# Kernel tuning notes

Hardware: AMD Instinct MI355X
Metric: run time of the kernel (lower is better)

## Reference

```python
import jax, jax.numpy as jnp
import numpy as np

N_NODES = 200000
D_IN = 256
D_OUT = 256
B = 4096
K1 = 25   # layer-1 fanout
K2 = 10   # layer-2 fanout
M = B * (1 + K2)  # layer-1 node set size: batch centers + their sampled neighbors


def setup_inputs() -> dict:
    key = jax.random.key(0)
    k1, k2, k3, k4, k5, k6 = jax.random.split(key, 6)
    features = jax.random.normal(k1, (N_NODES, D_IN), dtype=jnp.float32)
    # SageLayer weights: [out, 2*in] (concat path, gcn=False); small kaiming-like scale
    W1 = jax.random.normal(k2, (D_OUT, 2 * D_IN), dtype=jnp.float32) * 0.05
    W2 = jax.random.normal(k3, (D_OUT, 2 * D_OUT), dtype=jnp.float32) * 0.05
    nodes_batch = jax.random.randint(k4, (B,), 0, N_NODES, dtype=jnp.int64)
    neigh2 = jax.random.randint(k5, (B, K2), 0, N_NODES, dtype=jnp.int64)
    neigh1 = jax.random.randint(k6, (M, K1), 0, N_NODES, dtype=jnp.int64)
    return {"features": features, "W1": W1, "W2": W2,
            "nodes_batch": nodes_batch, "neigh2": neigh2, "neigh1": neigh1}


def reference(features, W1, W2, nodes_batch, neigh2, neigh1):
    # Layer-1 node set: centers first, then their sampled layer-2 neighbors.
    l1_nodes = jnp.concatenate([nodes_batch, neigh2.reshape(-1)])  # [M]
    # ---- layer 1: MEAN aggregate over K1 sampled neighbors (gather + mean) ----
    agg1 = jnp.mean(features[neigh1], axis=1)          # [M, K1, D_IN] -> [M, D_IN]
    self1 = features[l1_nodes]                         # [M, D_IN]
    # SageLayer: relu(W.mm(cat(self, agg).T)).T == relu(cat @ W.T)
    h1 = jax.nn.relu(jnp.concatenate([self1, agg1], axis=1) @ W1.T)  # [M, D_OUT]
    # ---- layer 2: centers are h1[:B]; neighbor embeddings are h1[B:] in blocks of K2 ----
    nb = nodes_batch.shape[0]
    agg2 = jnp.mean(h1[nb:].reshape(nb, -1, h1.shape[1]), axis=1)    # [B, D_OUT]
    h2 = jax.nn.relu(jnp.concatenate([h1[:nb], agg2], axis=1) @ W2.T)  # [B, D_OUT]
    return h2
```

## Files before the change

### kernel.cpp

```cpp
#include <hip/hip_runtime.h>
#include <hip/hip_bf16.h>

typedef __attribute__((ext_vector_type(8))) short bf16x8;
typedef __attribute__((ext_vector_type(4))) float f32x4;
typedef __attribute__((ext_vector_type(2))) float f32x2;

#define B_SZ   4096
#define K1     25
#define K2     10
#define M_L1   45056
#define D      256
#define K_DIM  512
#define N_NODES 200000

#define AS1 __attribute__((address_space(1)))
#define AS3 __attribute__((address_space(3)))

static __device__ __forceinline__ unsigned short f2bf(float f) {
    union { float f; unsigned u; } v; v.f = f;
    return (unsigned short)((v.u + 0x7fffu + ((v.u >> 16) & 1u)) >> 16);
}
static __device__ __forceinline__ float bf2f(unsigned short h) {
    union { unsigned u; float f; } v; v.u = ((unsigned)h) << 16;
    return v.f;
}

__global__ __launch_bounds__(256)
void convert_all(const float* __restrict__ f, unsigned* __restrict__ f8,
                 const float* __restrict__ W1, const float* __restrict__ W2,
                 unsigned short* __restrict__ W1b, unsigned short* __restrict__ W2b) {
    const size_t i = ((size_t)blockIdx.x * 256 + threadIdx.x) * 8;
    const float4 a = *(const float4*)(f + i);
    const float4 b = *(const float4*)(f + i + 4);
    unsigned u0 = 0, u1 = 0;
    u0 = __builtin_amdgcn_cvt_pk_fp8_f32(a.x, a.y, u0, false);
    u0 = __builtin_amdgcn_cvt_pk_fp8_f32(a.z, a.w, u0, true);
    u1 = __builtin_amdgcn_cvt_pk_fp8_f32(b.x, b.y, u1, false);
    u1 = __builtin_amdgcn_cvt_pk_fp8_f32(b.z, b.w, u1, true);
    uint2 r; r.x = u0; r.y = u1;
    *(uint2*)(f8 + (i >> 2)) = r;
    const int j = blockIdx.x * 256 + threadIdx.x;
    if (j < D * K_DIM) {
        W1b[j] = f2bf(W1[j]);
        W2b[j] = f2bf(W2[j]);
    }
}

__global__ __launch_bounds__(512)
void fused_l1(const float* __restrict__ feat,
              const unsigned* __restrict__ f8,
              const int* __restrict__ nodes_batch,
              const int* __restrict__ neigh2,
              const int* __restrict__ neigh1,
              const unsigned short* __restrict__ W,
              unsigned short* __restrict__ h1) {
    __shared__ unsigned short As[64 * 512];
    __shared__ unsigned short Bs[2][256 * 64];
    const int tid  = threadIdx.x;
    const int w    = tid >> 6, lane = tid & 63;
    const int quad = lane >> 4, l16 = lane & 15;
    const size_t row0 = (size_t)blockIdx.x * 64;

    const int srow   = lane >> 3;
    const int schunk = ((lane & 7) ^ srow) << 3;
    const unsigned short* bG = W + (size_t)srow * K_DIM + schunk;

    #pragma unroll
    for (int c = w; c < 32; c += 8)
        __builtin_amdgcn_global_load_lds(
            (const AS1 void*)(bG + (size_t)(c * 8) * K_DIM),
            (AS3 void*)(&Bs[0][c * 512]), 16, 0, 0);

    #pragma unroll 2
    for (int rr = 0; rr < 8; ++rr) {
        const int r = (w << 3) + rr;
        const int m = (int)row0 + r;
        const int self_node = (m < B_SZ) ? nodes_batch[m] : neigh2[m - B_SZ];
        const int* nb = neigh1 + (size_t)m * K1;
        int idxv = (lane < K1) ? nb[lane] : 0;
        const float4 s = *(const float4*)(feat + (size_t)self_node * D + (lane << 2));
        unsigned q[K1];
        #pragma unroll
        for (int j = 0; j < K1; ++j) {
            const int node = __shfl(idxv, j);
            q[j] = f8[(size_t)node * (D / 4) + lane];
        }
        float a0 = 0.f, a1 = 0.f, a2 = 0.f, a3 = 0.f;
        #pragma unroll
        for (int j = 0; j < K1; ++j) {
            const f32x2 lo = __builtin_amdgcn_cvt_pk_f32_fp8(q[j], false);
            const f32x2 hi = __builtin_amdgcn_cvt_pk_f32_fp8(q[j], true);
            a0 += lo.x; a1 += lo.y; a2 += hi.x; a3 += hi.y;
        }
        const float inv = 1.0f / (float)K1;
        const int e0 = lane << 2;
        const int p0 = (e0 >> 3) ^ (r & 7);
        *(ushort4*)&As[r * 512 + (p0 << 3) + (e0 & 7)] =
            make_ushort4(f2bf(s.x), f2bf(s.y), f2bf(s.z), f2bf(s.w));
        const int e1 = D + (lane << 2);
        const int p1 = (e1 >> 3) ^ (r & 7);
        *(ushort4*)&As[r * 512 + (p1 << 3) + (e1 & 7)] =
            make_ushort4(f2bf(a0 * inv), f2bf(a1 * inv), f2bf(a2 * inv), f2bf(a3 * inv));
    }

    asm volatile("s_waitcnt vmcnt(0)" ::: "memory");
    __syncthreads();

    const int wm = (w >> 2) << 5;
    const int wn = (w & 3) << 6;
    f32x4 acc[2][4];
    #pragma unroll
    for (int i = 0; i < 2; ++i)
        #pragma unroll
        for (int j = 0; j < 4; ++j)
            acc[i][j] = (f32x4){0.f, 0.f, 0.f, 0.f};

    for (int t = 0; t < 8; ++t) {
        if (t < 7) {
            #pragma unroll
            for (int c = w; c < 32; c += 8)
                __builtin_amdgcn_global_load_lds(
                    (const AS1 void*)(bG + (size_t)(c * 8) * K_DIM + ((t + 1) << 6)),
                    (AS3 void*)(&Bs[(t + 1) & 1][c * 512]), 16, 0, 0);
        }
        #pragma unroll
        for (int ks = 0; ks < 2; ++ks) {
            bf16x8 af[2], bfr[4];
            #pragma unroll
            for (int i = 0; i < 2; ++i) {
                const int row = wm + i * 16 + l16;
                const int ch  = (t << 3) + (ks << 2) + quad;
                af[i] = *(const bf16x8*)&As[row * 512 + ((ch ^ (row & 7)) << 3)];
            }
            #pragma unroll
            for (int i = 0; i < 4; ++i) {
                const int row = wn + i * 16 + l16;
                bfr[i] = *(const bf16x8*)&Bs[t & 1][row * 64 + ((((ks << 2) + quad) ^ (l16 & 7)) << 3)];
            }
            #pragma unroll
            for (int mi = 0; mi < 2; ++mi)
                #pragma unroll
                for (int ni = 0; ni < 4; ++ni)
                    acc[mi][ni] = __builtin_amdgcn_mfma_f32_16x16x32_bf16(
                        af[mi], bfr[ni], acc[mi][ni], 0, 0, 0);
        }
        asm volatile("s_waitcnt vmcnt(0)" ::: "memory");
        __syncthreads();
    }

    #pragma unroll
    for (int mi = 0; mi < 2; ++mi)
        #pragma unroll
        for (int ni = 0; ni < 4; ++ni)
            #pragma unroll
            for (int rg = 0; rg < 4; ++rg) {
                const size_t gm = row0 + wm + mi * 16 + quad * 4 + rg;
                const size_t gn = (size_t)wn + ni * 16 + l16;
                float v = acc[mi][ni][rg];
                v = v > 0.f ? v : 0.f;
                h1[gm * D + gn] = f2bf(v);
            }
}

__global__ __launch_bounds__(256)
void fused_l2(const unsigned short* __restrict__ h1,
              const unsigned short* __restrict__ W,
              float* __restrict__ out) {
    __shared__ unsigned short As[16 * 512];
    __shared__ unsigned short Bs[2][256 * 64];
    const int tid  = threadIdx.x;
    const int w    = tid >> 6, lane = tid & 63;
    const int quad = lane >> 4, l16 = lane & 15;
    const size_t row0 = (size_t)blockIdx.x * 16;

    const int srow   = lane >> 3;
    const int schunk = ((lane & 7) ^ srow) << 3;
    const unsigned short* bG = W + (size_t)srow * K_DIM + schunk;

    #pragma unroll
    for (int c = w; c < 32; c += 4)
        __builtin_amdgcn_global_load_lds(
            (const AS1 void*)(bG + (size_t)(c * 8) * K_DIM),
            (AS3 void*)(&Bs[0][c * 512]), 16, 0, 0);

    #pragma unroll
    for (int rr = 0; rr < 4; ++rr) {
        const int r = (w << 2) + rr;
        const size_t b = row0 + r;
        const ushort4 sv = *(const ushort4*)&h1[b * D + (lane << 2)];
        float a0 = 0.f, a1 = 0.f, a2 = 0.f, a3 = 0.f;
        #pragma unroll
        for (int k = 0; k < K2; ++k) {
            const ushort4 v = *(const ushort4*)&h1[(size_t)(B_SZ + b * K2 + k) * D + (lane << 2)];
            a0 += bf2f(v.x); a1 += bf2f(v.y); a2 += bf2f(v.z); a3 += bf2f(v.w);
        }
        const float inv = 1.0f / (float)K2;
        const int e0 = lane << 2;
        const int p0 = (e0 >> 3) ^ (r & 7);
        *(ushort4*)&As[r * 512 + (p0 << 3) + (e0 & 7)] = sv;
        const int e1 = D + (lane << 2);
        const int p1 = (e1 >> 3) ^ (r & 7);
        *(ushort4*)&As[r * 512 + (p1 << 3) + (e1 & 7)] =
            make_ushort4(f2bf(a0 * inv), f2bf(a1 * inv), f2bf(a2 * inv), f2bf(a3 * inv));
    }

    asm volatile("s_waitcnt vmcnt(0)" ::: "memory");
    __syncthreads();

    const int wn = w << 6;
    f32x4 acc[4];
    #pragma unroll
    for (int j = 0; j < 4; ++j) acc[j] = (f32x4){0.f, 0.f, 0.f, 0.f};

    for (int t = 0; t < 8; ++t) {
        if (t < 7) {
            #pragma unroll
            for (int c = w; c < 32; c += 4)
                __builtin_amdgcn_global_load_lds(
                    (const AS1 void*)(bG + (size_t)(c * 8) * K_DIM + ((t + 1) << 6)),
                    (AS3 void*)(&Bs[(t + 1) & 1][c * 512]), 16, 0, 0);
        }
        #pragma unroll
        for (int ks = 0; ks < 2; ++ks) {
            const int ch = (t << 3) + (ks << 2) + quad;
            const bf16x8 af = *(const bf16x8*)&As[l16 * 512 + ((ch ^ (l16 & 7)) << 3)];
            bf16x8 bfr[4];
            #pragma unroll
            for (int i = 0; i < 4; ++i) {
                const int row = wn + i * 16 + l16;
                bfr[i] = *(const bf16x8*)&Bs[t & 1][row * 64 + ((((ks << 2) + quad) ^ (l16 & 7)) << 3)];
            }
            #pragma unroll
            for (int ni = 0; ni < 4; ++ni)
                acc[ni] = __builtin_amdgcn_mfma_f32_16x16x32_bf16(af, bfr[ni], acc[ni], 0, 0, 0);
        }
        asm volatile("s_waitcnt vmcnt(0)" ::: "memory");
        __syncthreads();
    }

    #pragma unroll
    for (int ni = 0; ni < 4; ++ni)
        #pragma unroll
        for (int rg = 0; rg < 4; ++rg) {
            const size_t gm = row0 + quad * 4 + rg;
            const size_t gn = (size_t)wn + ni * 16 + l16;
            float v = acc[ni][rg];
            out[gm * D + gn] = v > 0.f ? v : 0.f;
        }
}

extern "C" void kernel_launch(void* const* d_in, const int* in_sizes, int n_in,
                              void* d_out, int out_size, void* d_ws, size_t ws_size,
                              hipStream_t stream) {
    const float* feat        = (const float*)d_in[0];
    const float* W1          = (const float*)d_in[1];
    const float* W2          = (const float*)d_in[2];
    const int*   nodes_batch = (const int*)d_in[3];
    const int*   neigh2      = (const int*)d_in[4];
    const int*   neigh1      = (const int*)d_in[5];
    float* out = (float*)d_out;

    char* ws = (char*)d_ws;
    unsigned*       f8  = (unsigned*)(ws);
    unsigned short* h1  = (unsigned short*)(ws + 51200000);
    unsigned short* W1b = (unsigned short*)(ws + 51200000 + 23068672);
    unsigned short* W2b = (unsigned short*)(ws + 51200000 + 23068672 + 262144);

    convert_all<<<25000, 256, 0, stream>>>(feat, f8, W1, W2, W1b, W2b);
    fused_l1<<<M_L1 / 64, 512, 0, stream>>>(feat, f8, nodes_batch, neigh2, neigh1, W1b, h1);
    fused_l2<<<B_SZ / 16, 256, 0, stream>>>(h1, W2b, out);
}
```

Before: 365.4 us.

## Load weight fragments directly into registers, drop LDS staging and shrink L1 tile

Both fused kernels now read W fragments straight from global memory into registers with a two-stage register double buffer, removing the LDS B-tile, the global_load_lds copies and the per-k-step barriers. Layer 1 also halves its row tile from 64 to 32, cutting LDS to 32 KB and doubling the grid, and both kernels get launch_bounds minimum-occupancy hints. The aim is higher occupancy so the latency-bound neighbor gather is better hidden. The cost is more register pressure and repeated global/L2 reads of W across warps and blocks, since it is no longer shared through LDS.

```diff
diff --git a/kernel.cpp b/kernel.cpp
--- a/kernel.cpp
+++ b/kernel.cpp
@@ -12,9 +12,6 @@
 #define D      256
 #define K_DIM  512
 #define N_NODES 200000
-
-#define AS1 __attribute__((address_space(1)))
-#define AS3 __attribute__((address_space(3)))
 
 static __device__ __forceinline__ unsigned short f2bf(float f) {
     union { float f; unsigned u; } v; v.f = f;
@@ -46,7 +43,7 @@
     }
 }
 
-__global__ __launch_bounds__(512)
+__global__ __launch_bounds__(512, 4)
 void fused_l1(const float* __restrict__ feat,
               const unsigned* __restrict__ f8,
               const int* __restrict__ nodes_batch,
@@ -54,26 +51,26 @@
               const int* __restrict__ neigh1,
               const unsigned short* __restrict__ W,
               unsigned short* __restrict__ h1) {
-    __shared__ unsigned short As[64 * 512];
-    __shared__ unsigned short Bs[2][256 * 64];
+    __shared__ unsigned short As[32 * 512];
     const int tid  = threadIdx.x;
     const int w    = tid >> 6, lane = tid & 63;
     const int quad = lane >> 4, l16 = lane & 15;
-    const size_t row0 = (size_t)blockIdx.x * 64;
-
-    const int srow   = lane >> 3;
-    const int schunk = ((lane & 7) ^ srow) << 3;
-    const unsigned short* bG = W + (size_t)srow * K_DIM + schunk;
-
-    #pragma unroll
-    for (int c = w; c < 32; c += 8)
-        __builtin_amdgcn_global_load_lds(
-            (const AS1 void*)(bG + (size_t)(c * 8) * K_DIM),
-            (AS3 void*)(&Bs[0][c * 512]), 16, 0, 0);
+    const int wm   = (w >> 2) << 4;
+    const int wn   = (w & 3) << 6;
+    const size_t row0 = (size_t)blockIdx.x * 32;
+
+    const unsigned short* bBase = W + (size_t)(wn + l16) * K_DIM + (quad << 3);
+
+    bf16x8 bp[2][8];
+    #pragma unroll
+    for (int ks = 0; ks < 2; ++ks)
+        #pragma unroll
+        for (int i = 0; i < 4; ++i)
+            bp[0][ks * 4 + i] = *(const bf16x8*)(bBase + (size_t)(i * 16) * K_DIM + ks * 32);
 
     #pragma unroll 2
-    for (int rr = 0; rr < 8; ++rr) {
-        const int r = (w << 3) + rr;
+    for (int rr = 0; rr < 4; ++rr) {
+        const int r = (w << 2) + rr;
         const int m = (int)row0 + r;
         const int self_node = (m < B_SZ) ? nodes_batch[m] : neigh2[m - B_SZ];
         const int* nb = neigh1 + (size_t)m * K1;
@@ -103,87 +100,67 @@
             make_ushort4(f2bf(a0 * inv), f2bf(a1 * inv), f2bf(a2 * inv), f2bf(a3 * inv));
     }
 
-    asm volatile("s_waitcnt vmcnt(0)" ::: "memory");
     __syncthreads();
 
-    const int wm = (w >> 2) << 5;
-    const int wn = (w & 3) << 6;
-    f32x4 acc[2][4];
-    #pragma unroll
-    for (int i = 0; i < 2; ++i)
-        #pragma unroll
-        for (int j = 0; j < 4; ++j)
-            acc[i][j] = (f32x4){0.f, 0.f, 0.f, 0.f};
-
+    f32x4 acc[4];
+    #pragma unroll
+    for (int j = 0; j < 4; ++j) acc[j] = (f32x4){0.f, 0.f, 0.f, 0.f};
+
+    #pragma unroll
     for (int t = 0; t < 8; ++t) {
         if (t < 7) {
             #pragma unroll
-            for (int c = w; c < 32; c += 8)
-                __builtin_amdgcn_global_load_lds(
-                    (const AS1 void*)(bG + (size_t)(c * 8) * K_DIM + ((t + 1) << 6)),
-                    (AS3 void*)(&Bs[(t + 1) & 1][c * 512]), 16, 0, 0);
+            for (int ks = 0; ks < 2; ++ks)
+                #pragma unroll
+                for (int i = 0; i < 4; ++i)
+                    bp[(t + 1) & 1][ks * 4 + i] =
+                        *(const bf16x8*)(bBase + (size_t)(i * 16) * K_DIM + (t + 1) * 64 + ks * 32);
         }
         #pragma unroll
         for (int ks = 0; ks < 2; ++ks) {
-            bf16x8 af[2], bfr[4];
-            #pragma unroll
-            for (int i = 0; i < 2; ++i) {
-                const int row = wm + i * 16 + l16;
-                const int ch  = (t << 3) + (ks << 2) + quad;
-                af[i] = *(const bf16x8*)&As[row * 512 + ((ch ^ (row & 7)) << 3)];
-            }
-            #pragma unroll
-            for (int i = 0; i < 4; ++i) {
-                const int row = wn + i * 16 + l16;
-                bfr[i] = *(const bf16x8*)&Bs[t & 1][row * 64 + ((((ks << 2) + quad) ^ (l16 & 7)) << 3)];
-            }
-            #pragma unroll
-            for (int mi = 0; mi < 2; ++mi)
-                #pragma unroll
-                for (int ni = 0; ni < 4; ++ni)
-                    acc[mi][ni] = __builtin_amdgcn_mfma_f32_16x16x32_bf16(
-                        af[mi], bfr[ni], acc[mi][ni], 0, 0, 0);
-        }
-        asm volatile("s_waitcnt vmcnt(0)" ::: "memory");
-        __syncthreads();
-    }
-
-    #pragma unroll
-    for (int mi = 0; mi < 2; ++mi)
-        #pragma unroll
-        for (int ni = 0; ni < 4; ++ni)
-            #pragma unroll
-            for (int rg = 0; rg < 4; ++rg) {
-                const size_t gm = row0 + wm + mi * 16 + quad * 4 + rg;
-                const size_t gn = (size_t)wn + ni * 16 + l16;
-                float v = acc[mi][ni][rg];
-                v = v > 0.f ? v : 0.f;
-                h1[gm * D + gn] = f2bf(v);
-            }
-}
-
-__global__ __launch_bounds__(256)
+            const int row = wm + l16;
+            const int ch  = (t << 3) + (ks << 2) + quad;
+            const bf16x8 af = *(const bf16x8*)&As[row * 512 + ((ch ^ (row & 7)) << 3)];
+            #pragma unroll
+            for (int ni = 0; ni < 4; ++ni)
+                acc[ni] = __builtin_amdgcn_mfma_f32_16x16x32_bf16(
+                    af, bp[t & 1][ks * 4 + ni], acc[ni], 0, 0, 0);
+        }
+    }
+
+    #pragma unroll
+    for (int ni = 0; ni < 4; ++ni)
+        #pragma unroll
+        for (int rg = 0; rg < 4; ++rg) {
+            const size_t gm = row0 + wm + quad * 4 + rg;
+            const size_t gn = (size_t)wn + ni * 16 + l16;
+            float v = acc[ni][rg];
+            v = v > 0.f ? v : 0.f;
+            h1[gm * D + gn] = f2bf(v);
+        }
+}
+
+__global__ __launch_bounds__(256, 4)
 void fused_l2(const unsigned short* __restrict__ h1,
               const unsigned short* __restrict__ W,
               float* __restrict__ out) {
     __shared__ unsigned short As[16 * 512];
-    __shared__ unsigned short Bs[2][256 * 64];
     const int tid  = threadIdx.x;
     const int w    = tid >> 6, lane = tid & 63;
     const int quad = lane >> 4, l16 = lane & 15;
+    const int wn   = w << 6;
     const size_t row0 = (size_t)blockIdx.x * 16;
 
-    const int srow   = lane >> 3;
-    const int schunk = ((lane & 7) ^ srow) << 3;
-    const unsigned short* bG = W + (size_t)srow * K_DIM + schunk;
-
-    #pragma unroll
-    for (int c = w; c < 32; c += 4)
-        __builtin_amdgcn_global_load_lds(
-            (const AS1 void*)(bG + (size_t)(c * 8) * K_DIM),
-            (AS3 void*)(&Bs[0][c * 512]), 16, 0, 0);
-
-    #pragma unroll
+    const unsigned short* bBase = W + (size_t)(wn + l16) * K_DIM + (quad << 3);
+
+    bf16x8 bp[2][8];
+    #pragma unroll
+    for (int ks = 0; ks < 2; ++ks)
+        #pragma unroll
+        for (int i = 0; i < 4; ++i)
+            bp[0][ks * 4 + i] = *(const bf16x8*)(bBase + (size_t)(i * 16) * K_DIM + ks * 32);
+
+    #pragma unroll 2
     for (int rr = 0; rr < 4; ++rr) {
         const int r = (w << 2) + rr;
         const size_t b = row0 + r;
@@ -204,38 +181,32 @@
             make_ushort4(f2bf(a0 * inv), f2bf(a1 * inv), f2bf(a2 * inv), f2bf(a3 * inv));
     }
 
-    asm volatile("s_waitcnt vmcnt(0)" ::: "memory");
     __syncthreads();
 
-    const int wn = w << 6;
     f32x4 acc[4];
     #pragma unroll
     for (int j = 0; j < 4; ++j) acc[j] = (f32x4){0.f, 0.f, 0.f, 0.f};
 
+    #pragma unroll
     for (int t = 0; t < 8; ++t) {
         if (t < 7) {
             #pragma unroll
-            for (int c = w; c < 32; c += 4)
-                __builtin_amdgcn_global_load_lds(
-                    (const AS1 void*)(bG + (size_t)(c * 8) * K_DIM + ((t + 1) << 6)),
-                    (AS3 void*)(&Bs[(t + 1) & 1][c * 512]), 16, 0, 0);
+            for (int ks = 0; ks < 2; ++ks)
+                #pragma unroll
+                for (int i = 0; i < 4; ++i)
+                    bp[(t + 1) & 1][ks * 4 + i] =
+                        *(const bf16x8*)(bBase + (size_t)(i * 16) * K_DIM + (t + 1) * 64 + ks * 32);
         }
         #pragma unroll
         for (int ks = 0; ks < 2; ++ks) {
-            const int ch = (t << 3) + (ks << 2) + quad;
-            const bf16x8 af = *(const bf16x8*)&As[l16 * 512 + ((ch ^ (l16 & 7)) << 3)];
-            bf16x8 bfr[4];
-            #pragma unroll
-            for (int i = 0; i < 4; ++i) {
-                const int row = wn + i * 16 + l16;
-                bfr[i] = *(const bf16x8*)&Bs[t & 1][row * 64 + ((((ks << 2) + quad) ^ (l16 & 7)) << 3)];
-            }
+            const int row = l16;
+            const int ch  = (t << 3) + (ks << 2) + quad;
+            const bf16x8 af = *(const bf16x8*)&As[row * 512 + ((ch ^ (row & 7)) << 3)];
             #pragma unroll
             for (int ni = 0; ni < 4; ++ni)
-                acc[ni] = __builtin_amdgcn_mfma_f32_16x16x32_bf16(af, bfr[ni], acc[ni], 0, 0, 0);
-        }
-        asm volatile("s_waitcnt vmcnt(0)" ::: "memory");
-        __syncthreads();
+                acc[ni] = __builtin_amdgcn_mfma_f32_16x16x32_bf16(
+                    af, bp[t & 1][ks * 4 + ni], acc[ni], 0, 0, 0);
+        }
     }
 
     #pragma unroll
@@ -267,6 +238,6 @@
     unsigned short* W2b = (unsigned short*)(ws + 51200000 + 23068672 + 262144);
 
     convert_all<<<25000, 256, 0, stream>>>(feat, f8, W1, W2, W1b, W2b);
-    fused_l1<<<M_L1 / 64, 512, 0, stream>>>(feat, f8, nodes_batch, neigh2, neigh1, W1b, h1);
+    fused_l1<<<M_L1 / 32, 512, 0, stream>>>(feat, f8, nodes_batch, neigh2, neigh1, W1b, h1);
     fused_l2<<<B_SZ / 16, 256, 0, stream>>>(h1, W2b, out);
 }
```

Result: slower. 441.5 us (+20.8%).
